# Kernel optimization log

Hardware: AMD Instinct MI355X
Metric: run time of the kernel (lower is better)

The kernel has to match this reference:

```python
import jax, jax.numpy as jnp
import numpy as np

# state_composition -> (modality, length); slices are consecutive offsets into D_state
COMP = [("joint_pos", 64), ("joint_vel", 64), ("eef_pose", 32), ("force", 32)]
NUM_EMB = 32   # num_embodiments
HID = 512      # hidden_size
EMB = 1024     # embed_dim
B, T = 16, 32


def setup_inputs() -> dict:
    key = jax.random.key(0)
    ks = iter(jax.random.split(key, 64))
    D = sum(L for _, L in COMP)
    inp = {
        "state_btD": jax.random.normal(next(ks), (B, T, D), jnp.float32),
        "embodiment_id_bt1": jax.random.randint(next(ks), (B, T, 1), 0, NUM_EMB, dtype=jnp.int64),
    }
    for m, L in COMP:
        inp[f"W1_{m}"] = 0.02 * jax.random.normal(next(ks), (NUM_EMB, L, HID), jnp.float32)
        inp[f"b1_{m}"] = jnp.zeros((NUM_EMB, HID), jnp.float32)
        inp[f"W2_{m}"] = 0.02 * jax.random.normal(next(ks), (NUM_EMB, HID, EMB), jnp.float32)
        inp[f"b2_{m}"] = jnp.zeros((NUM_EMB, EMB), jnp.float32)
        inp[f"te_{m}"] = 0.02 * jax.random.normal(next(ks), (1, 1, EMB), jnp.float32)
    return inp


def _cat_mlp(x, cat, W1, b1, W2, b2):
    # x: (N, in_dim), cat: (N,) int ids. Mirrors CategorySpecificMLP:
    # per-token weight gather W[cat] then bmm (here einsum over the token axis).
    h = jax.nn.relu(jnp.einsum("ni,nih->nh", x, W1[cat]) + b1[cat])
    return jnp.einsum("nh,nhe->ne", h, W2[cat]) + b2[cat]


def reference(state_btD, embodiment_id_bt1,
              W1_joint_pos, b1_joint_pos, W2_joint_pos, b2_joint_pos, te_joint_pos,
              W1_joint_vel, b1_joint_vel, W2_joint_vel, b2_joint_vel, te_joint_vel,
              W1_eef_pose, b1_eef_pose, W2_eef_pose, b2_eef_pose, te_eef_pose,
              W1_force, b1_force, W2_force, b2_force, te_force):
    Bv, Tv, D = state_btD.shape
    # expand (B,1,1) -> (B,T,1) if needed, then flatten to per-token ids
    cat = jnp.broadcast_to(embodiment_id_bt1, (Bv, Tv, 1)).reshape(Bv * Tv)
    params = [
        (W1_joint_pos, b1_joint_pos, W2_joint_pos, b2_joint_pos, te_joint_pos),
        (W1_joint_vel, b1_joint_vel, W2_joint_vel, b2_joint_vel, te_joint_vel),
        (W1_eef_pose, b1_eef_pose, W2_eef_pose, b2_eef_pose, te_eef_pose),
        (W1_force, b1_force, W2_force, b2_force, te_force),
    ]
    toks = []
    off = 0
    for (m, L), (W1, b1, W2, b2, te) in zip(COMP, params):
        x = state_btD[..., off:off + L].reshape(Bv * Tv, L)
        off += L
        z = _cat_mlp(x, cat, W1, b1, W2, b2) + te.reshape(EMB)
        toks.append(z.reshape(Bv, Tv, 1, EMB))
    return jnp.concatenate(toks, axis=2)  # (B, T, M, embed_dim)
```

## Files before the change

### kernel.cpp

```cpp
#include <hip/hip_runtime.h>

#define NCAT 32
#define NTOK 512
#define HID  512
#define EMB  1024
#define DSTATE 192
#define CHUNK 32
#define MAXW 48


__global__ __launch_bounds__(512) void bucket_kernel(
    const int* __restrict__ ids, int* __restrict__ cnt, int* __restrict__ nW,
    int* __restrict__ work, int* __restrict__ toklist)
{
    __shared__ int scnt[NCAT];
    const int tid = threadIdx.x;
    if (tid < NCAT) scnt[tid] = 0;
    __syncthreads();
    const int c = ids[tid];
    const int pos = atomicAdd(&scnt[c], 1);
    toklist[c * NTOK + pos] = tid;
    __syncthreads();
    if (tid == 0) {
        int n1 = 0;
        for (int cc = 0; cc < NCAT; ++cc) {
            const int n = scnt[cc];
            cnt[cc] = n;
            for (int ch = 0; ch * CHUNK < n; ++ch) work[n1++] = cc | (ch << 8);
        }
        nW[0] = n1;
    }
}

__device__ __forceinline__ void async_copy16(void* lds_dst, const void* g_src) {
    __builtin_amdgcn_global_load_lds(
        (__attribute__((address_space(1))) void*)(g_src),
        (__attribute__((address_space(3))) void*)(lds_dst),
        16, 0, 0);
}

__global__ __launch_bounds__(256, 1) void fused_kernel(
    const float* __restrict__ state,
    const int* __restrict__ cnt, const int* __restrict__ toklist,
    const int* __restrict__ nW, const int* __restrict__ work,
    const float* __restrict__ W1_0, const float* __restrict__ W1_1,
    const float* __restrict__ W1_2, const float* __restrict__ W1_3,
    const float* __restrict__ b1_0, const float* __restrict__ b1_1,
    const float* __restrict__ b1_2, const float* __restrict__ b1_3,
    const float* __restrict__ W2_0, const float* __restrict__ W2_1,
    const float* __restrict__ W2_2, const float* __restrict__ W2_3,
    const float* __restrict__ b2_0, const float* __restrict__ b2_1,
    const float* __restrict__ b2_2, const float* __restrict__ b2_3,
    const float* __restrict__ te_0, const float* __restrict__ te_1,
    const float* __restrict__ te_2, const float* __restrict__ te_3,
    float* __restrict__ out)
{
    const int slot = blockIdx.x, mod = blockIdx.y, z = blockIdx.z;
    if (slot >= nW[0]) return;
    const int ent = work[slot];
    const int cat = ent & 255, chunk = ent >> 8;
    const int nC = cnt[cat];
    const int start = chunk * CHUNK;
    int nThis = nC - start;
    if (nThis > CHUNK) nThis = CHUNK;
    const int tid = threadIdx.x;
    const int tg = tid >> 6;
    const int cg = tid & 63;

    const int L   = (mod < 2) ? 64 : 32;
    const int off = (mod == 0) ? 0 : (mod == 1) ? 64 : (mod == 2) ? 128 : 160;

    __shared__ float sX[64 * 32];
    __shared__ float sH[512 * 32];
    __shared__ float wbuf[3][8 * 512];
    __shared__ int sTok[CHUNK];

    if (tid < CHUNK) sTok[tid] = (tid < nThis) ? toklist[cat * NTOK + start + tid] : 0;
    __syncthreads();

    {
        const int tt = tid & 31, kg = tid >> 5;
        const int rpk = L >> 3;
        const float* src = state + (size_t)sTok[tt] * DSTATE + off + kg * rpk;
        const bool ok = tt < nThis;
        for (int j = 0; j < (rpk >> 2); ++j) {
            float4 v = make_float4(0.f, 0.f, 0.f, 0.f);
            if (ok) v = ((const float4*)src)[j];
            const int k0 = kg * rpk + (j << 2);
            sX[(k0 + 0) * 32 + tt] = v.x;
            sX[(k0 + 1) * 32 + tt] = v.y;
            sX[(k0 + 2) * 32 + tt] = v.z;
            sX[(k0 + 3) * 32 + tt] = v.w;
        }
    }
    __syncthreads();

    const float* W1 = (mod == 0) ? W1_0 : (mod == 1) ? W1_1 : (mod == 2) ? W1_2 : W1_3;
    const float* b1 = (mod == 0) ? b1_0 : (mod == 1) ? b1_1 : (mod == 2) ? b1_2 : b1_3;
    const float* W1c = W1 + (size_t)cat * L * HID + 2 * tid;

    float2 hacc[32];
#pragma unroll
    for (int t = 0; t < 32; ++t) hacc[t] = make_float2(0.f, 0.f);

#pragma unroll 4
    for (int k = 0; k < L; ++k) {
        const float2 w = *(const float2*)(W1c + (size_t)k * HID);
        const float4* xp = (const float4*)(sX + k * 32);
#pragma unroll
        for (int q = 0; q < 8; ++q) {
            const float4 x4 = xp[q];
            hacc[4*q+0].x += x4.x * w.x; hacc[4*q+0].y += x4.x * w.y;
            hacc[4*q+1].x += x4.y * w.x; hacc[4*q+1].y += x4.y * w.y;
            hacc[4*q+2].x += x4.z * w.x; hacc[4*q+2].y += x4.z * w.y;
            hacc[4*q+3].x += x4.w * w.x; hacc[4*q+3].y += x4.w * w.y;
        }
    }
    {
        const float2 bb = *(const float2*)(b1 + cat * HID + 2 * tid);
        float4* s4 = (float4*)sH;
        const int key = tid & 7;
        const int r0 = 2 * tid, r1 = 2 * tid + 1;
#pragma unroll
        for (int q = 0; q < 8; ++q) {
            float4 v0, v1;
            v0.x = fmaxf(hacc[4*q+0].x + bb.x, 0.f);
            v0.y = fmaxf(hacc[4*q+1].x + bb.x, 0.f);
            v0.z = fmaxf(hacc[4*q+2].x + bb.x, 0.f);
            v0.w = fmaxf(hacc[4*q+3].x + bb.x, 0.f);
            v1.x = fmaxf(hacc[4*q+0].y + bb.y, 0.f);
            v1.y = fmaxf(hacc[4*q+1].y + bb.y, 0.f);
            v1.z = fmaxf(hacc[4*q+2].y + bb.y, 0.f);
            v1.w = fmaxf(hacc[4*q+3].y + bb.y, 0.f);
            s4[r0 * 8 + (q ^ key)] = v0;
            s4[r1 * 8 + (q ^ key)] = v1;
        }
    }

    const float* W2 = (mod == 0) ? W2_0 : (mod == 1) ? W2_1 : (mod == 2) ? W2_2 : W2_3;
    const float* Wc = W2 + (size_t)cat * (HID * EMB) + z * 512;

#define STAGE_TILE(T, wb) do {                                                  \
        const float* gsrc_ = Wc + (size_t)((T) * 8 + (tid >> 7)) * EMB          \
                             + ((tid & 127) << 2);                              \
        float* ldst_ = (wb) + ((tid >> 6) << 8);                                \
        async_copy16(ldst_,        gsrc_);                                      \
        async_copy16(ldst_ + 1024, gsrc_ + 2 * EMB);                            \
        async_copy16(ldst_ + 2048, gsrc_ + 4 * EMB);                            \
        async_copy16(ldst_ + 3072, gsrc_ + 6 * EMB);                            \
    } while (0)

    STAGE_TILE(0, wbuf[0]);
    STAGE_TILE(1, wbuf[1]);
    asm volatile("s_waitcnt vmcnt(4) lgkmcnt(0)" ::: "memory");
    __builtin_amdgcn_s_barrier();
    asm volatile("" ::: "memory");
    __builtin_amdgcn_sched_barrier(0);

    const int hbase = tg << 3;
    const int tq0   = tg << 1;
    const int wcol  = cg << 2;
    const bool act  = hbase < nThis;

    float4 a0[8], a1[8];
#pragma unroll
    for (int i = 0; i < 8; ++i) {
        a0[i] = make_float4(0.f, 0.f, 0.f, 0.f);
        a1[i] = make_float4(0.f, 0.f, 0.f, 0.f);
    }

    int bcur = 0;
#pragma unroll 1
    for (int T = 0; T < 64; ++T) {
        int b2i = bcur + 2; if (b2i >= 3) b2i -= 3;
        if (T + 2 < 64) STAGE_TILE(T + 2, wbuf[b2i]);
        if (act) {
            const float* wb = wbuf[bcur];
            const int kb = T << 3;
#pragma unroll
            for (int r = 0; r < 8; ++r) {
                const int k  = kb + r;
                const int kk = (k >> 1) & 7;
                const float4 h0 = ((const float4*)sH)[k * 8 + (tq0 ^ kk)];
                const float4 h1 = ((const float4*)sH)[k * 8 + ((tq0 + 1) ^ kk)];
                const float4 w0 = *(const float4*)(wb + r * 512 + wcol);
                const float4 w1 = *(const float4*)(wb + r * 512 + 256 + wcol);
#define FMA2(i, s) a0[i].x += (s)*w0.x; a0[i].y += (s)*w0.y;                    \
                   a0[i].z += (s)*w0.z; a0[i].w += (s)*w0.w;                    \
                   a1[i].x += (s)*w1.x; a1[i].y += (s)*w1.y;                    \
                   a1[i].z += (s)*w1.z; a1[i].w += (s)*w1.w;
                FMA2(0, h0.x) FMA2(1, h0.y) FMA2(2, h0.z) FMA2(3, h0.w)
                FMA2(4, h1.x) FMA2(5, h1.y) FMA2(6, h1.z) FMA2(7, h1.w)
#undef FMA2
            }
        }
        if (T < 63) {
            if (T + 2 < 64) { asm volatile("s_waitcnt vmcnt(4)" ::: "memory"); }
            else            { asm volatile("s_waitcnt vmcnt(0)" ::: "memory"); }
            __builtin_amdgcn_s_barrier();
            asm volatile("" ::: "memory");
            __builtin_amdgcn_sched_barrier(0);
        }
        bcur = bcur + 1; if (bcur == 3) bcur = 0;
    }
#undef STAGE_TILE

    const float* b2 = (mod == 0) ? b2_0 : (mod == 1) ? b2_1 : (mod == 2) ? b2_2 : b2_3;
    const float* te = (mod == 0) ? te_0 : (mod == 1) ? te_1 : (mod == 2) ? te_2 : te_3;
    const int colA = z * 512 + wcol;
    const int colB = colA + 256;
    const float4 bA = *(const float4*)(b2 + cat * EMB + colA);
    const float4 bB = *(const float4*)(b2 + cat * EMB + colB);
    const float4 tA = *(const float4*)(te + colA);
    const float4 tB = *(const float4*)(te + colB);
#pragma unroll
    for (int i = 0; i < 8; ++i) {
        const int t = hbase + i;
        if (t >= nThis) break;
        float* op = out + (size_t)(sTok[t] * 4 + mod) * EMB;
        *(float4*)(op + colA) = make_float4(a0[i].x + bA.x + tA.x,
                                            a0[i].y + bA.y + tA.y,
                                            a0[i].z + bA.z + tA.z,
                                            a0[i].w + bA.w + tA.w);
        *(float4*)(op + colB) = make_float4(a1[i].x + bB.x + tB.x,
                                            a1[i].y + bB.y + tB.y,
                                            a1[i].z + bB.z + tB.z,
                                            a1[i].w + bB.w + tB.w);
    }
}

extern "C" void kernel_launch(void* const* d_in, const int* in_sizes, int n_in,
                              void* d_out, int out_size, void* d_ws, size_t ws_size,
                              hipStream_t stream) {
    const float* state = (const float*)d_in[0];
    const int*   ids   = (const int*)d_in[1];
    const float *W1[4], *b1[4], *W2[4], *b2[4], *te[4];
    for (int m = 0; m < 4; ++m) {
        W1[m] = (const float*)d_in[2 + 5 * m + 0];
        b1[m] = (const float*)d_in[2 + 5 * m + 1];
        W2[m] = (const float*)d_in[2 + 5 * m + 2];
        b2[m] = (const float*)d_in[2 + 5 * m + 3];
        te[m] = (const float*)d_in[2 + 5 * m + 4];
    }
    char* ws = (char*)d_ws;
    int*   cnt     = (int*)ws;
    int*   nW      = (int*)(ws + 128);
    int*   work    = (int*)(ws + 256);
    int*   toklist = (int*)(ws + 1024);
    float* out     = (float*)d_out;

    bucket_kernel<<<1, 512, 0, stream>>>(ids, cnt, nW, work, toklist);
    fused_kernel<<<dim3(MAXW, 4, 2), 256, 0, stream>>>(
        state, cnt, toklist, nW, work,
        W1[0], W1[1], W1[2], W1[3],
        b1[0], b1[1], b1[2], b1[3],
        W2[0], W2[1], W2[2], W2[3],
        b2[0], b2[1], b2[2], b2[3],
        te[0], te[1], te[2], te[3], out);
}
```

Baseline: 328.6 us.

## Load W2 tiles directly into registers with double buffering instead of LDS staging

Replaces the triple-buffered async global-to-LDS staging of W2 tiles, with its per-tile barriers, by direct per-thread float4 global loads into register double buffers, overlapped with FMAs through sched_barriers. This drops 48KB of shared memory and raises the occupancy hint to 2 blocks per CU. The cost is that each of the 4 thread groups now loads the same W2 row data from global memory/cache, four times the load traffic of before, and register pressure rises with 64 extra float4 buffer registers. Inactive thread groups skip the loads entirely.

```diff
diff --git a/kernel.cpp b/kernel.cpp
--- a/kernel.cpp
+++ b/kernel.cpp
@@ -32,14 +32,7 @@
     }
 }
 
-__device__ __forceinline__ void async_copy16(void* lds_dst, const void* g_src) {
-    __builtin_amdgcn_global_load_lds(
-        (__attribute__((address_space(1))) void*)(g_src),
-        (__attribute__((address_space(3))) void*)(lds_dst),
-        16, 0, 0);
-}
-
-__global__ __launch_bounds__(256, 1) void fused_kernel(
+__global__ __launch_bounds__(256, 2) void fused_kernel(
     const float* __restrict__ state,
     const int* __restrict__ cnt, const int* __restrict__ toklist,
     const int* __restrict__ nW, const int* __restrict__ work,
@@ -72,7 +65,6 @@
 
     __shared__ float sX[64 * 32];
     __shared__ float sH[512 * 32];
-    __shared__ float wbuf[3][8 * 512];
     __shared__ int sTok[CHUNK];
 
     if (tid < CHUNK) sTok[tid] = (tid < nThis) ? toklist[cat * NTOK + start + tid] : 0;
@@ -136,30 +128,14 @@
             s4[r1 * 8 + (q ^ key)] = v1;
         }
     }
+    __syncthreads();
 
     const float* W2 = (mod == 0) ? W2_0 : (mod == 1) ? W2_1 : (mod == 2) ? W2_2 : W2_3;
-    const float* Wc = W2 + (size_t)cat * (HID * EMB) + z * 512;
-
-#define STAGE_TILE(T, wb) do {                                                  \
-        const float* gsrc_ = Wc + (size_t)((T) * 8 + (tid >> 7)) * EMB          \
-                             + ((tid & 127) << 2);                              \
-        float* ldst_ = (wb) + ((tid >> 6) << 8);                                \
-        async_copy16(ldst_,        gsrc_);                                      \
-        async_copy16(ldst_ + 1024, gsrc_ + 2 * EMB);                            \
-        async_copy16(ldst_ + 2048, gsrc_ + 4 * EMB);                            \
-        async_copy16(ldst_ + 3072, gsrc_ + 6 * EMB);                            \
-    } while (0)
-
-    STAGE_TILE(0, wbuf[0]);
-    STAGE_TILE(1, wbuf[1]);
-    asm volatile("s_waitcnt vmcnt(4) lgkmcnt(0)" ::: "memory");
-    __builtin_amdgcn_s_barrier();
-    asm volatile("" ::: "memory");
-    __builtin_amdgcn_sched_barrier(0);
+    const int wcol = cg << 2;
+    const float* Wc = W2 + (size_t)cat * (HID * EMB) + z * 512 + wcol;
 
     const int hbase = tg << 3;
     const int tq0   = tg << 1;
-    const int wcol  = cg << 2;
     const bool act  = hbase < nThis;
 
     float4 a0[8], a1[8];
@@ -169,41 +145,55 @@
         a1[i] = make_float4(0.f, 0.f, 0.f, 0.f);
     }
 
-    int bcur = 0;
-#pragma unroll 1
-    for (int T = 0; T < 64; ++T) {
-        int b2i = bcur + 2; if (b2i >= 3) b2i -= 3;
-        if (T + 2 < 64) STAGE_TILE(T + 2, wbuf[b2i]);
-        if (act) {
-            const float* wb = wbuf[bcur];
-            const int kb = T << 3;
-#pragma unroll
-            for (int r = 0; r < 8; ++r) {
-                const int k  = kb + r;
-                const int kk = (k >> 1) & 7;
-                const float4 h0 = ((const float4*)sH)[k * 8 + (tq0 ^ kk)];
-                const float4 h1 = ((const float4*)sH)[k * 8 + ((tq0 + 1) ^ kk)];
-                const float4 w0 = *(const float4*)(wb + r * 512 + wcol);
-                const float4 w1 = *(const float4*)(wb + r * 512 + 256 + wcol);
+#define LOAD_TILE(T, ba, bb) do {                                               \
+        const float* pt_ = Wc + (size_t)(T) * 8 * EMB;                          \
+        _Pragma("unroll")                                                       \
+        for (int r_ = 0; r_ < 8; ++r_) {                                        \
+            ba[r_] = *(const float4*)(pt_ + (size_t)r_ * EMB);                  \
+            bb[r_] = *(const float4*)(pt_ + (size_t)r_ * EMB + 256);            \
+        }                                                                       \
+    } while (0)
+
 #define FMA2(i, s) a0[i].x += (s)*w0.x; a0[i].y += (s)*w0.y;                    \
                    a0[i].z += (s)*w0.z; a0[i].w += (s)*w0.w;                    \
                    a1[i].x += (s)*w1.x; a1[i].y += (s)*w1.y;                    \
                    a1[i].z += (s)*w1.z; a1[i].w += (s)*w1.w;
-                FMA2(0, h0.x) FMA2(1, h0.y) FMA2(2, h0.z) FMA2(3, h0.w)
-                FMA2(4, h1.x) FMA2(5, h1.y) FMA2(6, h1.z) FMA2(7, h1.w)
+
+#define FMA_TILE(T, ba, bb) do {                                                \
+        _Pragma("unroll")                                                       \
+        for (int r_ = 0; r_ < 8; ++r_) {                                        \
+            const int k_  = (T) * 8 + r_;                                       \
+            const int kk_ = (k_ >> 1) & 7;                                      \
+            const float4 h0 = ((const float4*)sH)[k_ * 8 + (tq0 ^ kk_)];        \
+            const float4 h1 = ((const float4*)sH)[k_ * 8 + ((tq0 + 1) ^ kk_)];  \
+            const float4 w0 = ba[r_];                                           \
+            const float4 w1 = bb[r_];                                           \
+            FMA2(0, h0.x) FMA2(1, h0.y) FMA2(2, h0.z) FMA2(3, h0.w)             \
+            FMA2(4, h1.x) FMA2(5, h1.y) FMA2(6, h1.z) FMA2(7, h1.w)             \
+        }                                                                       \
+    } while (0)
+
+    if (act) {
+        float4 Aa[8], Ab[8], Ba[8], Bb[8];
+        LOAD_TILE(0, Aa, Ab);
+        __builtin_amdgcn_sched_barrier(0);
+#pragma unroll 1
+        for (int T = 0; T < 62; T += 2) {
+            LOAD_TILE(T + 1, Ba, Bb);
+            __builtin_amdgcn_sched_barrier(0);
+            FMA_TILE(T, Aa, Ab);
+            LOAD_TILE(T + 2, Aa, Ab);
+            __builtin_amdgcn_sched_barrier(0);
+            FMA_TILE(T + 1, Ba, Bb);
+        }
+        LOAD_TILE(63, Ba, Bb);
+        __builtin_amdgcn_sched_barrier(0);
+        FMA_TILE(62, Aa, Ab);
+        FMA_TILE(63, Ba, Bb);
+    }
+#undef LOAD_TILE
+#undef FMA_TILE
 #undef FMA2
-            }
-        }
-        if (T < 63) {
-            if (T + 2 < 64) { asm volatile("s_waitcnt vmcnt(4)" ::: "memory"); }
-            else            { asm volatile("s_waitcnt vmcnt(0)" ::: "memory"); }
-            __builtin_amdgcn_s_barrier();
-            asm volatile("" ::: "memory");
-            __builtin_amdgcn_sched_barrier(0);
-        }
-        bcur = bcur + 1; if (bcur == 3) bcur = 0;
-    }
-#undef STAGE_TILE
 
     const float* b2 = (mod == 0) ? b2_0 : (mod == 1) ? b2_1 : (mod == 2) ? b2_2 : b2_3;
     const float* te = (mod == 0) ? te_0 : (mod == 1) ? te_1 : (mod == 2) ? te_2 : te_3;
```

Result: slower. 546.9 us (+66.4%).

## Halve shared memory by splitting hidden-state staging to fit two blocks per CU

Applied to the files above, without the earlier changes.

Shrinks shared memory from roughly 100KB to 80KB by holding only half of the hidden activations in LDS at a time and overlaying the input tile with the weight ring buffer. The second half of H is written after the first 32 K-tiles, and launch bounds are raised to two blocks per CU to improve occupancy and latency hiding. In exchange, 64 hacc registers stay live across the first half of the GEMM loop, which risks register spills under the tighter 2-block register budget. It also adds an extra barrier, and token ids are re-read from global memory at the output stage.

```diff
diff --git a/kernel.cpp b/kernel.cpp
--- a/kernel.cpp
+++ b/kernel.cpp
@@ -39,7 +39,7 @@
         16, 0, 0);
 }
 
-__global__ __launch_bounds__(256, 1) void fused_kernel(
+__global__ __launch_bounds__(256, 2) void fused_kernel(
     const float* __restrict__ state,
     const int* __restrict__ cnt, const int* __restrict__ toklist,
     const int* __restrict__ nW, const int* __restrict__ work,
@@ -70,18 +70,17 @@
     const int L   = (mod < 2) ? 64 : 32;
     const int off = (mod == 0) ? 0 : (mod == 1) ? 64 : (mod == 2) ? 128 : 160;
 
-    __shared__ float sX[64 * 32];
-    __shared__ float sH[512 * 32];
-    __shared__ float wbuf[3][8 * 512];
-    __shared__ int sTok[CHUNK];
-
-    if (tid < CHUNK) sTok[tid] = (tid < nThis) ? toklist[cat * NTOK + start + tid] : 0;
-    __syncthreads();
+    __shared__ __align__(16) float smem[20480];
+    float* const sH  = smem;
+    float* const wbB = smem + 8192;
+    float* const sX  = smem + 8192;
 
     {
         const int tt = tid & 31, kg = tid >> 5;
         const int rpk = L >> 3;
-        const float* src = state + (size_t)sTok[tt] * DSTATE + off + kg * rpk;
+        int tok = 0;
+        if (tt < nThis) tok = toklist[cat * NTOK + start + tt];
+        const float* src = state + (size_t)tok * DSTATE + off + kg * rpk;
         const bool ok = tt < nThis;
         for (int j = 0; j < (rpk >> 2); ++j) {
             float4 v = make_float4(0.f, 0.f, 0.f, 0.f);
@@ -118,50 +117,49 @@
     }
     {
         const float2 bb = *(const float2*)(b1 + cat * HID + 2 * tid);
-        float4* s4 = (float4*)sH;
-        const int key = tid & 7;
-        const int r0 = 2 * tid, r1 = 2 * tid + 1;
-#pragma unroll
-        for (int q = 0; q < 8; ++q) {
-            float4 v0, v1;
-            v0.x = fmaxf(hacc[4*q+0].x + bb.x, 0.f);
-            v0.y = fmaxf(hacc[4*q+1].x + bb.x, 0.f);
-            v0.z = fmaxf(hacc[4*q+2].x + bb.x, 0.f);
-            v0.w = fmaxf(hacc[4*q+3].x + bb.x, 0.f);
-            v1.x = fmaxf(hacc[4*q+0].y + bb.y, 0.f);
-            v1.y = fmaxf(hacc[4*q+1].y + bb.y, 0.f);
-            v1.z = fmaxf(hacc[4*q+2].y + bb.y, 0.f);
-            v1.w = fmaxf(hacc[4*q+3].y + bb.y, 0.f);
-            s4[r0 * 8 + (q ^ key)] = v0;
-            s4[r1 * 8 + (q ^ key)] = v1;
-        }
-    }
+#pragma unroll
+        for (int t = 0; t < 32; ++t) {
+            hacc[t].x = fmaxf(hacc[t].x + bb.x, 0.f);
+            hacc[t].y = fmaxf(hacc[t].y + bb.y, 0.f);
+        }
+    }
+
+#define WRITE_SH() do {                                                         \
+        float4* s4_ = (float4*)sH;                                              \
+        const int key_ = tid & 7;                                               \
+        const int r0_ = (2 * tid) & 255;                                        \
+        _Pragma("unroll")                                                       \
+        for (int q_ = 0; q_ < 8; ++q_) {                                        \
+            float4 v0_, v1_;                                                    \
+            v0_.x = hacc[4*q_+0].x; v0_.y = hacc[4*q_+1].x;                     \
+            v0_.z = hacc[4*q_+2].x; v0_.w = hacc[4*q_+3].x;                     \
+            v1_.x = hacc[4*q_+0].y; v1_.y = hacc[4*q_+1].y;                     \
+            v1_.z = hacc[4*q_+2].y; v1_.w = hacc[4*q_+3].y;                     \
+            s4_[(r0_ + 0) * 8 + (q_ ^ key_)] = v0_;                             \
+            s4_[(r0_ + 1) * 8 + (q_ ^ key_)] = v1_;                             \
+        }                                                                       \
+    } while (0)
+
+    if (tid < 128) WRITE_SH();
+    __syncthreads();
 
     const float* W2 = (mod == 0) ? W2_0 : (mod == 1) ? W2_1 : (mod == 2) ? W2_2 : W2_3;
     const float* Wc = W2 + (size_t)cat * (HID * EMB) + z * 512;
-
-#define STAGE_TILE(T, wb) do {                                                  \
+    const int wcol  = cg << 2;
+    const int hbase = tg << 3;
+    const int tq0   = tg << 1;
+    const bool act  = hbase < nThis;
+
+#define STAGE_TILE(T, wbase) do {                                               \
         const float* gsrc_ = Wc + (size_t)((T) * 8 + (tid >> 7)) * EMB          \
                              + ((tid & 127) << 2);                              \
-        float* ldst_ = (wb) + ((tid >> 6) << 8);                                \
+        float* ldst_ = (wbase) + ((tid >> 6) << 8);                             \
         async_copy16(ldst_,        gsrc_);                                      \
         async_copy16(ldst_ + 1024, gsrc_ + 2 * EMB);                            \
         async_copy16(ldst_ + 2048, gsrc_ + 4 * EMB);                            \
         async_copy16(ldst_ + 3072, gsrc_ + 6 * EMB);                            \
     } while (0)
 
-    STAGE_TILE(0, wbuf[0]);
-    STAGE_TILE(1, wbuf[1]);
-    asm volatile("s_waitcnt vmcnt(4) lgkmcnt(0)" ::: "memory");
-    __builtin_amdgcn_s_barrier();
-    asm volatile("" ::: "memory");
-    __builtin_amdgcn_sched_barrier(0);
-
-    const int hbase = tg << 3;
-    const int tq0   = tg << 1;
-    const int wcol  = cg << 2;
-    const bool act  = hbase < nThis;
-
     float4 a0[8], a1[8];
 #pragma unroll
     for (int i = 0; i < 8; ++i) {
@@ -169,41 +167,66 @@
         a1[i] = make_float4(0.f, 0.f, 0.f, 0.f);
     }
 
-    int bcur = 0;
-#pragma unroll 1
-    for (int T = 0; T < 64; ++T) {
-        int b2i = bcur + 2; if (b2i >= 3) b2i -= 3;
-        if (T + 2 < 64) STAGE_TILE(T + 2, wbuf[b2i]);
-        if (act) {
-            const float* wb = wbuf[bcur];
-            const int kb = T << 3;
-#pragma unroll
-            for (int r = 0; r < 8; ++r) {
-                const int k  = kb + r;
-                const int kk = (k >> 1) & 7;
-                const float4 h0 = ((const float4*)sH)[k * 8 + (tq0 ^ kk)];
-                const float4 h1 = ((const float4*)sH)[k * 8 + ((tq0 + 1) ^ kk)];
-                const float4 w0 = *(const float4*)(wb + r * 512 + wcol);
-                const float4 w1 = *(const float4*)(wb + r * 512 + 256 + wcol);
 #define FMA2(i, s) a0[i].x += (s)*w0.x; a0[i].y += (s)*w0.y;                    \
                    a0[i].z += (s)*w0.z; a0[i].w += (s)*w0.w;                    \
                    a1[i].x += (s)*w1.x; a1[i].y += (s)*w1.y;                    \
                    a1[i].z += (s)*w1.z; a1[i].w += (s)*w1.w;
-                FMA2(0, h0.x) FMA2(1, h0.y) FMA2(2, h0.z) FMA2(3, h0.w)
-                FMA2(4, h1.x) FMA2(5, h1.y) FMA2(6, h1.z) FMA2(7, h1.w)
-#undef FMA2
-            }
-        }
+
+#define COMP_TILE(T, wbase) do {                                                \
+        _Pragma("unroll")                                                       \
+        for (int r_ = 0; r_ < 8; ++r_) {                                        \
+            const int k_  = (T) * 8 + r_;                                       \
+            const int kk_ = (k_ >> 1) & 7;                                      \
+            const int kr_ = k_ & 255;                                           \
+            const float4 h0 = ((const float4*)sH)[kr_ * 8 + (tq0 ^ kk_)];       \
+            const float4 h1 = ((const float4*)sH)[kr_ * 8 + ((tq0 + 1) ^ kk_)]; \
+            const float4 w0 = *(const float4*)((wbase) + r_ * 512 + wcol);      \
+            const float4 w1 = *(const float4*)((wbase) + r_ * 512 + 256 + wcol);\
+            FMA2(0, h0.x) FMA2(1, h0.y) FMA2(2, h0.z) FMA2(3, h0.w)             \
+            FMA2(4, h1.x) FMA2(5, h1.y) FMA2(6, h1.z) FMA2(7, h1.w)             \
+        }                                                                       \
+    } while (0)
+
+    STAGE_TILE(0, wbB);
+    STAGE_TILE(1, wbB + 4096);
+    asm volatile("s_waitcnt vmcnt(4)" ::: "memory");
+    __builtin_amdgcn_s_barrier();
+    __builtin_amdgcn_sched_barrier(0);
+
+    int bcur = 0;
+#pragma unroll 1
+    for (int T = 0; T < 32; ++T) {
+        int bnx = bcur + 2; if (bnx >= 3) bnx -= 3;
+        STAGE_TILE(T + 2, wbB + bnx * 4096);
+        if (act) COMP_TILE(T, wbB + bcur * 4096);
+        asm volatile("s_waitcnt vmcnt(4)" ::: "memory");
+        __builtin_amdgcn_s_barrier();
+        __builtin_amdgcn_sched_barrier(0);
+        bcur += 1; if (bcur == 3) bcur = 0;
+    }
+
+    if (tid >= 128) WRITE_SH();
+    asm volatile("s_waitcnt lgkmcnt(0)" ::: "memory");
+    __builtin_amdgcn_s_barrier();
+    __builtin_amdgcn_sched_barrier(0);
+
+#pragma unroll 1
+    for (int T = 32; T < 64; ++T) {
+        int bnx = bcur + 2; if (bnx >= 3) bnx -= 3;
+        if (T + 2 < 64) STAGE_TILE(T + 2, wbB + bnx * 4096);
+        if (act) COMP_TILE(T, wbB + bcur * 4096);
         if (T < 63) {
             if (T + 2 < 64) { asm volatile("s_waitcnt vmcnt(4)" ::: "memory"); }
             else            { asm volatile("s_waitcnt vmcnt(0)" ::: "memory"); }
             __builtin_amdgcn_s_barrier();
-            asm volatile("" ::: "memory");
             __builtin_amdgcn_sched_barrier(0);
         }
-        bcur = bcur + 1; if (bcur == 3) bcur = 0;
+        bcur += 1; if (bcur == 3) bcur = 0;
     }
 #undef STAGE_TILE
+#undef COMP_TILE
+#undef FMA2
+#undef WRITE_SH
 
     const float* b2 = (mod == 0) ? b2_0 : (mod == 1) ? b2_1 : (mod == 2) ? b2_2 : b2_3;
     const float* te = (mod == 0) ? te_0 : (mod == 1) ? te_1 : (mod == 2) ? te_2 : te_3;
@@ -217,7 +240,8 @@
     for (int i = 0; i < 8; ++i) {
         const int t = hbase + i;
         if (t >= nThis) break;
-        float* op = out + (size_t)(sTok[t] * 4 + mod) * EMB;
+        const int tok = toklist[cat * NTOK + start + t];
+        float* op = out + (size_t)(tok * 4 + mod) * EMB;
         *(float4*)(op + colA) = make_float4(a0[i].x + bA.x + tA.x,
                                             a0[i].y + bA.y + tA.y,
                                             a0[i].z + bA.z + tA.z,
```

Measured after the change: 343.9 us. 1.05x slower.
